# Performance work log

Hardware: AMD Instinct MI355X
Metric: run time of the kernel (lower is better)

The kernel has to match this reference:

```python
import jax, jax.numpy as jnp
import numpy as np

N = 50000      # nodes
E = 800000     # edges
NF = 128       # node_features
BF = 16        # bond_features
H = 4          # heads
C = 32         # hidden_size (per-head out channels)
HC = H * C     # 128 == NF, so all GAT layers share weight shape
DEPTH = 5
NEG_SLOPE = 0.2


def _sanitize(t):
    return jnp.nan_to_num(t, nan=0.0, posinf=1000.0, neginf=-1000.0)


def setup_inputs() -> dict:
    key = jax.random.key(0)
    ks = jax.random.split(key, 12)
    s = 0.1
    x = jax.random.normal(ks[0], (N, NF), jnp.float32)
    edge_index = jax.random.randint(ks[1], (2, E), 0, N, dtype=jnp.int32)
    edge_attr = jax.random.uniform(ks[2], (E, BF), jnp.float32)
    W = jax.random.normal(ks[3], (DEPTH, NF, HC), jnp.float32) * s
    att_src = jax.random.normal(ks[4], (DEPTH, H, C), jnp.float32) * s
    att_dst = jax.random.normal(ks[5], (DEPTH, H, C), jnp.float32) * s
    We = jax.random.normal(ks[6], (DEPTH, BF, HC), jnp.float32) * s
    att_edge = jax.random.normal(ks[7], (DEPTH, H, C), jnp.float32) * s
    b = jnp.zeros((DEPTH, HC), jnp.float32)
    Wout = jax.random.normal(ks[8], (NF + HC, C), jnp.float32) * s
    bout = jnp.zeros((C,), jnp.float32)
    return {"x": x, "edge_index": edge_index, "edge_attr": edge_attr,
            "W": W, "att_src": att_src, "att_dst": att_dst,
            "We": We, "att_edge": att_edge, "b": b,
            "Wout": Wout, "bout": bout}


def _gat_layer(h, s2, d2, ea, W_l, as_l, ad_l, We_l, ae_l, b_l):
    # h: [N, in_dim]; s2/d2: [E+N] edges incl. self loops; ea: [E+N, BF]
    xp = (h @ W_l).reshape(N, H, C)                     # lin(x), view per-head
    a_s = jnp.sum(xp * as_l, axis=-1)                   # [N, H]
    a_d = jnp.sum(xp * ad_l, axis=-1)                   # [N, H]
    ee = (ea @ We_l).reshape(-1, H, C)                  # lin_edge(edge_attr)
    a_e = jnp.sum(ee * ae_l, axis=-1)                   # [E+N, H]
    alpha = jax.nn.leaky_relu(a_s[s2] + a_d[d2] + a_e, NEG_SLOPE)
    # segment softmax over edges grouped by destination node
    m = jax.ops.segment_max(alpha, d2, num_segments=N)  # every node has a self loop -> finite
    ex = jnp.exp(alpha - m[d2])
    den = jax.ops.segment_sum(ex, d2, num_segments=N)
    coef = ex / (den[d2] + 1e-16)                       # [E+N, H]
    out = jax.ops.segment_sum(coef[:, :, None] * xp[s2], d2, num_segments=N)
    return out.reshape(N, HC) + b_l


def reference(x, edge_index, edge_attr, W, att_src, att_dst, We, att_edge, b, Wout, bout):
    src, dst = edge_index[0], edge_index[1]
    # add self loops with fill_value='mean': self-loop attr = mean of incoming edge_attr
    deg = jax.ops.segment_sum(jnp.ones((E,), edge_attr.dtype), dst, num_segments=N)
    sl_attr = jax.ops.segment_sum(edge_attr, dst, num_segments=N) / jnp.maximum(deg, 1.0)[:, None]
    ea = jnp.concatenate([edge_attr, sl_attr], axis=0)          # [E+N, BF]
    loop = jnp.arange(N, dtype=src.dtype)
    s2 = jnp.concatenate([src, loop])
    d2 = jnp.concatenate([dst, loop])

    h = _sanitize(x)
    for l in range(DEPTH):
        h = _gat_layer(h, s2, d2, ea, W[l], att_src[l], att_dst[l], We[l], att_edge[l], b[l])
        h = jax.nn.relu(h)            # dropout is a no-op in eval mode
        h = _sanitize(h)
    h_cat = jnp.concatenate([x, h], axis=1)             # [N, NF+HC]
    out = jax.nn.relu(h_cat @ Wout + bout)
    return _sanitize(out)
```

## Files before the change

### kernel.cpp

```cpp
#include <hip/hip_runtime.h>

#define NN 50000
#define NE 800000
#define NF 128
#define BF 16
#define NH 4
#define HC 128
#define CC 32
#define DEPTH 5
#define NEG 0.2f
#define NPART 256
#define PTILE 4096

typedef __attribute__((ext_vector_type(8))) short bf16x8;
typedef __attribute__((ext_vector_type(4))) float f32x4;

__device__ inline unsigned short f2bf(float f) {
  union { float f; unsigned u; } v; v.f = f;
  unsigned r = v.u + 0x7fff + ((v.u >> 16) & 1);
  return (unsigned short)(r >> 16);
}
__device__ inline float bf2f(unsigned short u) {
  union { unsigned u; float f; } v; v.u = (unsigned)u << 16; return v.f;
}

__global__ void k_count(const int* __restrict__ dst, int* __restrict__ deg) {
  int e = blockIdx.x * 256 + threadIdx.x;
  if (e < NE) atomicAdd(&deg[dst[e]], 1);
}

__global__ void k_partial(const int* __restrict__ deg, int* __restrict__ bsum) {
  __shared__ int s[256];
  int t = threadIdx.x;
  int i = blockIdx.x * 256 + t;
  s[t] = (i < NN) ? deg[i] : 0;
  __syncthreads();
  for (int d = 128; d > 0; d >>= 1) {
    if (t < d) s[t] += s[t + d];
    __syncthreads();
  }
  if (t == 0) bsum[blockIdx.x] = s[0];
}

__global__ void k_scan_top(int* __restrict__ bsum, int nb) {
  if (threadIdx.x == 0 && blockIdx.x == 0) {
    int run = 0;
    for (int i = 0; i < nb; ++i) { int v = bsum[i]; bsum[i] = run; run += v; }
  }
}

__global__ void k_scan_write(const int* __restrict__ deg, const int* __restrict__ bsum,
                             int* __restrict__ offs) {
  __shared__ int s[256];
  int t = threadIdx.x;
  int i = blockIdx.x * 256 + t;
  int v = (i < NN) ? deg[i] : 0;
  s[t] = v;
  __syncthreads();
  for (int d = 1; d < 256; d <<= 1) {
    int x = (t >= d) ? s[t - d] : 0;
    __syncthreads();
    s[t] += x;
    __syncthreads();
  }
  if (i < NN) offs[i] = bsum[blockIdx.x] + s[t] - v;
  if (i == 0) offs[NN] = NE;
}

__global__ void k_initcur(const int* __restrict__ offs, int* __restrict__ cur) {
  int i = blockIdx.x * 256 + threadIdx.x;
  if (i < NN) cur[i] = offs[i];
}

__global__ __launch_bounds__(256) void k_p0(const int* __restrict__ edst, int* __restrict__ pcnt) {
  __shared__ int lc[NPART];
  int t = threadIdx.x;
  lc[t] = 0;
  __syncthreads();
  int base = blockIdx.x * PTILE;
#pragma unroll
  for (int j = 0; j < PTILE / 256; ++j) {
    int e = base + t + j * 256;
    if (e < NE) atomicAdd(&lc[edst[e] >> 8], 1);
  }
  __syncthreads();
  if (lc[t]) atomicAdd(&pcnt[t], lc[t]);
}

__global__ void k_pscan(const int* __restrict__ pcnt, int* __restrict__ pbase,
                        int* __restrict__ pcur) {
  __shared__ int s[NPART];
  int t = threadIdx.x;
  int v = pcnt[t];
  s[t] = v;
  __syncthreads();
  for (int d = 1; d < NPART; d <<= 1) {
    int x = (t >= d) ? s[t - d] : 0;
    __syncthreads();
    s[t] += x;
    __syncthreads();
  }
  int ex = s[t] - v;
  pbase[t] = ex;
  pcur[t] = ex;
  if (t == NPART - 1) pbase[NPART] = s[NPART - 1];
}

__global__ __launch_bounds__(256) void k_p1(const int* __restrict__ edst,
                                            int* __restrict__ pcur,
                                            int2* __restrict__ staging) {
  __shared__ int lc[NPART];
  __shared__ int lbase[NPART];
  __shared__ int lrank[NPART];
  int t = threadIdx.x;
  lc[t] = 0;
  __syncthreads();
  int base = blockIdx.x * PTILE;
  int myd[PTILE / 256];
#pragma unroll
  for (int j = 0; j < PTILE / 256; ++j) {
    int e = base + t + j * 256;
    int d = (e < NE) ? edst[e] : -1;
    myd[j] = d;
    if (d >= 0) atomicAdd(&lc[d >> 8], 1);
  }
  __syncthreads();
  if (lc[t]) lbase[t] = atomicAdd(&pcur[t], lc[t]);
  lrank[t] = 0;
  __syncthreads();
#pragma unroll
  for (int j = 0; j < PTILE / 256; ++j) {
    int d = myd[j];
    if (d >= 0) {
      int p = d >> 8;
      int r = atomicAdd(&lrank[p], 1);
      staging[lbase[p] + r] = make_int2(base + t + j * 256, d);
    }
  }
}

__global__ __launch_bounds__(256) void k_p2(const int2* __restrict__ staging,
                                            const int* __restrict__ pbase,
                                            int* __restrict__ cur,
                                            int* __restrict__ csr_eid) {
  int p = blockIdx.x;
  int s = pbase[p], e = pbase[p + 1];
  for (int i = s + threadIdx.x; i < e; i += 256) {
    int2 st = staging[i];
    int slot = atomicAdd(&cur[st.y], 1);
    csr_eid[slot] = st.x;
  }
}

__global__ void k_weff(const float* __restrict__ We, const float* __restrict__ ae,
                       float* __restrict__ weff) {
  int idx = threadIdx.x;
  if (idx >= DEPTH * BF * NH) return;
  int l = idx / (BF * NH);
  int r = idx - l * (BF * NH);
  int f = r >> 2, h = r & 3;
  const float* We_l = We + (size_t)l * BF * HC;
  const float* ae_l = ae + (size_t)l * NH * CC;
  float acc = 0.f;
  for (int c = 0; c < CC; ++c) acc += We_l[f * HC + h * CC + c] * ae_l[h * CC + c];
  weff[idx] = acc;
}

__global__ __launch_bounds__(256) void k_aeprep(const int* __restrict__ csr_eid,
                                                const int* __restrict__ esrc,
                                                const float* __restrict__ eattr,
                                                const float* __restrict__ weff,
                                                unsigned short* __restrict__ ae_csr,
                                                int* __restrict__ csr_src) {
  __shared__ float sw[DEPTH * BF * NH];
  int t = threadIdx.x;
  if (t < DEPTH * BF * NH) sw[t] = weff[t];
  __syncthreads();
  int i = blockIdx.x * 256 + t;
  if (i >= NE) return;
  int eid = csr_eid[i];
  csr_src[i] = esrc[eid];
  float at[16];
  const float4* ar = (const float4*)(eattr + (size_t)eid * BF);
#pragma unroll
  for (int q = 0; q < 4; ++q) {
    float4 v = ar[q];
    at[q * 4] = v.x; at[q * 4 + 1] = v.y; at[q * 4 + 2] = v.z; at[q * 4 + 3] = v.w;
  }
#pragma unroll
  for (int l = 0; l < DEPTH; ++l) {
    float a0 = 0.f, a1 = 0.f, a2 = 0.f, a3 = 0.f;
#pragma unroll
    for (int f = 0; f < BF; ++f) {
      float av = at[f];
      const float* wf = &sw[(l * BF + f) * NH];
      a0 += av * wf[0]; a1 += av * wf[1]; a2 += av * wf[2]; a3 += av * wf[3];
    }
    ushort4 u;
    u.x = f2bf(a0); u.y = f2bf(a1); u.z = f2bf(a2); u.w = f2bf(a3);
    ((ushort4*)ae_csr)[(size_t)l * NE + i] = u;
  }
}

__global__ void k_aeself(const unsigned short* __restrict__ ae_csr,
                         const int* __restrict__ offs,
                         unsigned short* __restrict__ ae_self) {
  int idx = blockIdx.x * 256 + threadIdx.x;
  if (idx >= NN * DEPTH) return;
  int l = idx / NN, n = idx - l * NN;
  int s = offs[n], e = offs[n + 1];
  const ushort4* base = (const ushort4*)ae_csr + (size_t)l * NE;
  float a0 = 0.f, a1 = 0.f, a2 = 0.f, a3 = 0.f;
  for (int i = s; i < e; ++i) {
    ushort4 u = base[i];
    a0 += bf2f(u.x); a1 += bf2f(u.y); a2 += bf2f(u.z); a3 += bf2f(u.w);
  }
  float inv = 1.0f / fmaxf((float)(e - s), 1.0f);
  ushort4 o;
  o.x = f2bf(a0 * inv); o.y = f2bf(a1 * inv); o.z = f2bf(a2 * inv); o.w = f2bf(a3 * inv);
  ((ushort4*)ae_self)[(size_t)l * NN + n] = o;
}

__global__ void k_x2bf(const float* __restrict__ x, unsigned short* __restrict__ xb) {
  int i = blockIdx.x * 256 + threadIdx.x;
  if (i >= NN * 32) return;
  float4 v = ((const float4*)x)[i];
  ushort4 u;
  u.x = f2bf(v.x); u.y = f2bf(v.y); u.z = f2bf(v.z); u.w = f2bf(v.w);
  ((ushort4*)xb)[i] = u;
}

__global__ void k_wprep(const float* __restrict__ W, unsigned short* __restrict__ Wt) {
  int idx = blockIdx.x * 256 + threadIdx.x;
  if (idx >= DEPTH * NF * HC) return;
  int l = idx >> 14;
  int rem = idx & 16383;
  int n = rem >> 7, k = rem & 127;
  Wt[(size_t)l * 16384 + (size_t)n * 128 + k] = f2bf(W[(size_t)l * 16384 + (size_t)k * 128 + n]);
}

__global__ __launch_bounds__(256) void k_gemm_mfma(const unsigned short* __restrict__ Ab,
                                                   const unsigned short* __restrict__ Wt,
                                                   const float* __restrict__ as_w,
                                                   const float* __restrict__ ad_w,
                                                   unsigned short* __restrict__ xpb,
                                                   float* __restrict__ a_s,
                                                   float* __restrict__ a_d) {
  __shared__ unsigned short cl[64][144];
  __shared__ float swS[128], dwS[128];
  int t = threadIdx.x;
  if (t < 128) { swS[t] = as_w[t]; dwS[t] = ad_w[t]; }
  int wv = t >> 6;
  int l = t & 63;
  int r0 = blockIdx.x * 64;
  int lk = (l >> 4) * 8;
  int c0 = wv * 32;
  f32x4 acc[4][2] = {};
#pragma unroll
  for (int ks = 0; ks < 4; ++ks) {
    int kb = ks * 32 + lk;
    bf16x8 bfr0 = *(const bf16x8*)&Wt[(size_t)(c0 + (l & 15)) * 128 + kb];
    bf16x8 bfr1 = *(const bf16x8*)&Wt[(size_t)(c0 + 16 + (l & 15)) * 128 + kb];
#pragma unroll
    for (int rt = 0; rt < 4; ++rt) {
      int row = r0 + rt * 16 + (l & 15);
      row = row < NN ? row : NN - 1;
      bf16x8 afr = *(const bf16x8*)&Ab[(size_t)row * 128 + kb];
      acc[rt][0] = __builtin_amdgcn_mfma_f32_16x16x32_bf16(afr, bfr0, acc[rt][0], 0, 0, 0);
      acc[rt][1] = __builtin_amdgcn_mfma_f32_16x16x32_bf16(afr, bfr1, acc[rt][1], 0, 0, 0);
    }
  }
#pragma unroll
  for (int rt = 0; rt < 4; ++rt) {
#pragma unroll
    for (int j = 0; j < 4; ++j) {
      int lr = rt * 16 + (l >> 4) * 4 + j;
      cl[lr][c0 + (l & 15)] = f2bf(acc[rt][0][j]);
      cl[lr][c0 + 16 + (l & 15)] = f2bf(acc[rt][1][j]);
    }
  }
  __syncthreads();
  int row = t >> 2;
  int grow = r0 + row;
  int p = t & 3;
  if (grow < NN) {
    uint4* dst = (uint4*)&xpb[(size_t)grow * 128];
#pragma unroll
    for (int q = 0; q < 4; ++q)
      dst[q * 4 + p] = *(uint4*)&cl[row][(q * 4 + p) * 8];
  }
  int hh = t & 3;
  int hc = hh * 32;
  float ps = 0.f, pd = 0.f;
#pragma unroll
  for (int q = 0; q < 4; ++q) {
    uint4 u = *(uint4*)&cl[row][hc + q * 8];
    const unsigned short* us = (const unsigned short*)&u;
#pragma unroll
    for (int k = 0; k < 8; ++k) {
      float xv = bf2f(us[k]);
      ps += xv * swS[hc + q * 8 + k];
      pd += xv * dwS[hc + q * 8 + k];
    }
  }
  if (grow < NN) {
    a_s[(size_t)grow * 4 + hh] = ps;
    a_d[(size_t)grow * 4 + hh] = pd;
  }
}

__global__ __launch_bounds__(256) void k_aggr(const unsigned short* __restrict__ xpb,
                                              const unsigned short* __restrict__ ae_l,
                                              const unsigned short* __restrict__ aeself_l,
                                              const float* __restrict__ a_s,
                                              const float* __restrict__ a_d,
                                              const int* __restrict__ csr_src,
                                              const int* __restrict__ offs,
                                              const float* __restrict__ b_l,
                                              unsigned short* __restrict__ hout) {
  int node = blockIdx.x * 4 + (threadIdx.x >> 6);
  if (node >= NN) return;
  int lane = threadIdx.x & 63;
  int q = lane & 15;
  int h = lane >> 4;
  int base = lane & 48;
  const ushort2* xp2 = (const ushort2*)xpb;
  int s = offs[node], e = offs[node + 1];
  float ad = a_d[(size_t)node * 4 + h];
  float vs = a_s[(size_t)node * 4 + h] + ad + bf2f(aeself_l[(size_t)node * 4 + h]);
  vs = vs > 0.f ? vs : NEG * vs;
  float es = __expf(fminf(vs, 60.f));
  ushort2 xs = xp2[(size_t)node * 64 + lane];
  float acc0 = es * bf2f(xs.x), acc1 = es * bf2f(xs.y);
  float den = es;
  for (int i = s; i < e; i += 16) {
    int cnt = e - i;
    int srcv = 0;
    float w = 0.f;
    if (q < cnt) {
      srcv = csr_src[i + q];
      float a = a_s[(size_t)srcv * 4 + h] + ad + bf2f(ae_l[(size_t)(i + q) * 4 + h]);
      a = a > 0.f ? a : NEG * a;
      w = __expf(fminf(a, 60.f));
    }
#pragma unroll 8
    for (int qq = 0; qq < 16; ++qq) {
      int sq = __shfl(srcv, base | qq);
      float wq = __shfl(w, base | qq);
      ushort2 xq = xp2[(size_t)sq * 64 + lane];
      den += wq;
      acc0 += wq * bf2f(xq.x);
      acc1 += wq * bf2f(xq.y);
    }
  }
  float2 b2 = ((const float2*)b_l)[lane];
  float inv = 1.0f / (den + 1e-16f);
  float o0 = fmaxf(acc0 * inv + b2.x, 0.f);
  float o1 = fmaxf(acc1 * inv + b2.y, 0.f);
  ushort2 ho;
  ho.x = f2bf(o0); ho.y = f2bf(o1);
  ((ushort2*)hout)[(size_t)node * 64 + lane] = ho;
}

__global__ __launch_bounds__(256) void k_final(const float* __restrict__ x,
                                               const unsigned short* __restrict__ h,
                                               const float* __restrict__ Wout, const float* __restrict__ bout,
                                               float* __restrict__ out) {
  __shared__ float4 wlds[2048];
  int t = threadIdx.x;
#pragma unroll
  for (int i = 0; i < 8; ++i) wlds[t + i * 256] = ((const float4*)Wout)[t + i * 256];
  __syncthreads();
  int tx = t & 7;
  int ty = t >> 3;
  int row0 = blockIdx.x * 64 + ty;
  int row1 = row0 + 32;
  bool v0 = row0 < NN, v1 = row1 < NN;
  const float4* x4 = (const float4*)x;
  const ushort4* h4 = (const ushort4*)h;
  float acc[2][4] = {};
  const float4 z = make_float4(0.f, 0.f, 0.f, 0.f);
#pragma unroll 4
  for (int k4 = 0; k4 < 32; ++k4) {
    float4 a0 = v0 ? x4[(size_t)row0 * 32 + k4] : z;
    float4 a1 = v1 ? x4[(size_t)row1 * 32 + k4] : z;
    float av0[4] = {a0.x, a0.y, a0.z, a0.w};
    float av1[4] = {a1.x, a1.y, a1.z, a1.w};
#pragma unroll
    for (int kk = 0; kk < 4; ++kk) {
      float4 w = wlds[(k4 * 4 + kk) * 8 + tx];
      acc[0][0] += av0[kk] * w.x; acc[0][1] += av0[kk] * w.y;
      acc[0][2] += av0[kk] * w.z; acc[0][3] += av0[kk] * w.w;
      acc[1][0] += av1[kk] * w.x; acc[1][1] += av1[kk] * w.y;
      acc[1][2] += av1[kk] * w.z; acc[1][3] += av1[kk] * w.w;
    }
  }
#pragma unroll 4
  for (int k4 = 0; k4 < 32; ++k4) {
    ushort4 u0 = v0 ? h4[(size_t)row0 * 32 + k4] : make_ushort4(0, 0, 0, 0);
    ushort4 u1 = v1 ? h4[(size_t)row1 * 32 + k4] : make_ushort4(0, 0, 0, 0);
    float av0[4] = {bf2f(u0.x), bf2f(u0.y), bf2f(u0.z), bf2f(u0.w)};
    float av1[4] = {bf2f(u1.x), bf2f(u1.y), bf2f(u1.z), bf2f(u1.w)};
#pragma unroll
    for (int kk = 0; kk < 4; ++kk) {
      float4 w = wlds[(128 + k4 * 4 + kk) * 8 + tx];
      acc[0][0] += av0[kk] * w.x; acc[0][1] += av0[kk] * w.y;
      acc[0][2] += av0[kk] * w.z; acc[0][3] += av0[kk] * w.w;
      acc[1][0] += av1[kk] * w.x; acc[1][1] += av1[kk] * w.y;
      acc[1][2] += av1[kk] * w.z; acc[1][3] += av1[kk] * w.w;
    }
  }
  float4 b4 = ((const float4*)bout)[tx];
  if (v0) {
    float4 o = make_float4(fmaxf(acc[0][0] + b4.x, 0.f), fmaxf(acc[0][1] + b4.y, 0.f),
                           fmaxf(acc[0][2] + b4.z, 0.f), fmaxf(acc[0][3] + b4.w, 0.f));
    ((float4*)out)[(size_t)row0 * 8 + tx] = o;
  }
  if (v1) {
    float4 o = make_float4(fmaxf(acc[1][0] + b4.x, 0.f), fmaxf(acc[1][1] + b4.y, 0.f),
                           fmaxf(acc[1][2] + b4.z, 0.f), fmaxf(acc[1][3] + b4.w, 0.f));
    ((float4*)out)[(size_t)row1 * 8 + tx] = o;
  }
}

extern "C" void kernel_launch(void* const* d_in, const int* in_sizes, int n_in,
                              void* d_out, int out_size, void* d_ws, size_t ws_size,
                              hipStream_t stream) {
  const float* x        = (const float*)d_in[0];
  const int*   eidx     = (const int*)d_in[1];
  const float* eattr    = (const float*)d_in[2];
  const float* W        = (const float*)d_in[3];
  const float* att_src  = (const float*)d_in[4];
  const float* att_dst  = (const float*)d_in[5];
  const float* We       = (const float*)d_in[6];
  const float* att_edge = (const float*)d_in[7];
  const float* b        = (const float*)d_in[8];
  const float* Wout     = (const float*)d_in[9];
  const float* bout     = (const float*)d_in[10];
  float* out = (float*)d_out;

  const int* esrc = eidx;
  const int* edst = eidx + NE;

  size_t off = 0;
  auto carve = [&](size_t bytes) {
    void* p = (char*)d_ws + off;
    off += (bytes + 255) & ~(size_t)255;
    return p;
  };
  unsigned short* h_buf   = (unsigned short*)carve((size_t)NN * HC * 2);
  unsigned short* xpb     = (unsigned short*)carve((size_t)NN * HC * 2);
  unsigned short* Wt      = (unsigned short*)carve((size_t)DEPTH * NF * HC * 2);
  unsigned short* ae_csr  = (unsigned short*)carve((size_t)DEPTH * NE * NH * 2);
  unsigned short* ae_self = (unsigned short*)carve((size_t)DEPTH * NN * NH * 2);
  float* a_s   = (float*)carve((size_t)NN * NH * 4);
  float* a_d   = (float*)carve((size_t)NN * NH * 4);
  float* weff  = (float*)carve((size_t)DEPTH * BF * NH * 4);
  int* deg  = (int*)carve((size_t)NN * 4);
  int* offs = (int*)carve((size_t)(NN + 1) * 4);
  int* cur  = (int*)carve((size_t)NN * 4);
  int2* staging = (int2*)carve((size_t)NE * 8);
  int* csr_eid = (int*)carve((size_t)NE * 4);
  int* csr_src = (int*)carve((size_t)NE * 4);
  int* pcnt  = (int*)carve((size_t)NPART * 4);
  int* pbase = (int*)carve((size_t)(NPART + 1) * 4);
  int* pcur  = (int*)carve((size_t)NPART * 4);
  int* bsum = (int*)carve(1024);

  const int nbN = (NN + 255) / 256;
  const int nbE = (NE + 255) / 256;
  const int nbP = (NE + PTILE - 1) / PTILE;

  hipMemsetAsync(deg, 0, (size_t)NN * 4, stream);
  hipMemsetAsync(pcnt, 0, (size_t)NPART * 4, stream);
  k_count<<<nbE, 256, 0, stream>>>(edst, deg);
  k_partial<<<nbN, 256, 0, stream>>>(deg, bsum);
  k_scan_top<<<1, 64, 0, stream>>>(bsum, nbN);
  k_scan_write<<<nbN, 256, 0, stream>>>(deg, bsum, offs);
  k_initcur<<<nbN, 256, 0, stream>>>(offs, cur);
  k_p0<<<nbP, 256, 0, stream>>>(edst, pcnt);
  k_pscan<<<1, NPART, 0, stream>>>(pcnt, pbase, pcur);
  k_p1<<<nbP, 256, 0, stream>>>(edst, pcur, staging);
  k_p2<<<NPART, 256, 0, stream>>>(staging, pbase, cur, csr_eid);
  k_weff<<<1, 320, 0, stream>>>(We, att_edge, weff);
  k_aeprep<<<nbE, 256, 0, stream>>>(csr_eid, esrc, eattr, weff, ae_csr, csr_src);
  k_aeself<<<(NN * DEPTH + 255) / 256, 256, 0, stream>>>(ae_csr, offs, ae_self);
  k_x2bf<<<(NN * 32 + 255) / 256, 256, 0, stream>>>(x, h_buf);
  k_wprep<<<(DEPTH * NF * HC + 255) / 256, 256, 0, stream>>>(W, Wt);

  for (int l = 0; l < DEPTH; ++l) {
    k_gemm_mfma<<<(NN + 63) / 64, 256, 0, stream>>>(h_buf, Wt + (size_t)l * NF * HC,
                                                    att_src + (size_t)l * NH * CC,
                                                    att_dst + (size_t)l * NH * CC,
                                                    xpb, a_s, a_d);
    k_aggr<<<(NN + 3) / 4, 256, 0, stream>>>(xpb,
                                             ae_csr + (size_t)l * NE * NH,
                                             ae_self + (size_t)l * NN * NH,
                                             a_s, a_d, csr_src, offs,
                                             b + (size_t)l * HC, h_buf);
  }
  k_final<<<(NN + 63) / 64, 256, 0, stream>>>(x, h_buf, Wout, bout, out);
}
```

Measured before the change: 484.0 us.

## Fuse CSR setup kernels, enlarge GEMM row tile, add nontemporal loads/stores in aggregation

Merges the degree count and partition histogram into one pass over destinations, and folds the cur initialisation into the scan-write kernel, which removes two launches and one read of the edge array. The MFMA GEMM now handles 128 rows per block instead of 64, reusing the weight fragments across more rows at the cost of more accumulator registers and LDS. The aggregation kernel uses nontemporal loads for the streamed CSR source and edge-attention arrays and a nontemporal packed store for the output, so that streaming data pollutes the cache less.

```diff
diff --git a/kernel.cpp b/kernel.cpp
--- a/kernel.cpp
+++ b/kernel.cpp
@@ -24,9 +24,25 @@
   union { unsigned u; float f; } v; v.u = (unsigned)u << 16; return v.f;
 }
 
-__global__ void k_count(const int* __restrict__ dst, int* __restrict__ deg) {
-  int e = blockIdx.x * 256 + threadIdx.x;
-  if (e < NE) atomicAdd(&deg[dst[e]], 1);
+__global__ __launch_bounds__(256) void k_cnt0(const int* __restrict__ edst,
+                                              int* __restrict__ deg,
+                                              int* __restrict__ pcnt) {
+  __shared__ int lc[NPART];
+  int t = threadIdx.x;
+  lc[t] = 0;
+  __syncthreads();
+  int base = blockIdx.x * PTILE;
+#pragma unroll
+  for (int j = 0; j < PTILE / 256; ++j) {
+    int e = base + t + j * 256;
+    if (e < NE) {
+      int d = edst[e];
+      atomicAdd(&deg[d], 1);
+      atomicAdd(&lc[d >> 8], 1);
+    }
+  }
+  __syncthreads();
+  if (lc[t]) atomicAdd(&pcnt[t], lc[t]);
 }
 
 __global__ void k_partial(const int* __restrict__ deg, int* __restrict__ bsum) {
@@ -50,7 +66,7 @@
 }
 
 __global__ void k_scan_write(const int* __restrict__ deg, const int* __restrict__ bsum,
-                             int* __restrict__ offs) {
+                             int* __restrict__ offs, int* __restrict__ cur) {
   __shared__ int s[256];
   int t = threadIdx.x;
   int i = blockIdx.x * 256 + t;
@@ -63,28 +79,12 @@
     s[t] += x;
     __syncthreads();
   }
-  if (i < NN) offs[i] = bsum[blockIdx.x] + s[t] - v;
+  if (i < NN) {
+    int o = bsum[blockIdx.x] + s[t] - v;
+    offs[i] = o;
+    cur[i] = o;
+  }
   if (i == 0) offs[NN] = NE;
-}
-
-__global__ void k_initcur(const int* __restrict__ offs, int* __restrict__ cur) {
-  int i = blockIdx.x * 256 + threadIdx.x;
-  if (i < NN) cur[i] = offs[i];
-}
-
-__global__ __launch_bounds__(256) void k_p0(const int* __restrict__ edst, int* __restrict__ pcnt) {
-  __shared__ int lc[NPART];
-  int t = threadIdx.x;
-  lc[t] = 0;
-  __syncthreads();
-  int base = blockIdx.x * PTILE;
-#pragma unroll
-  for (int j = 0; j < PTILE / 256; ++j) {
-    int e = base + t + j * 256;
-    if (e < NE) atomicAdd(&lc[edst[e] >> 8], 1);
-  }
-  __syncthreads();
-  if (lc[t]) atomicAdd(&pcnt[t], lc[t]);
 }
 
 __global__ void k_pscan(const int* __restrict__ pcnt, int* __restrict__ pbase,
@@ -246,23 +246,23 @@
                                                    unsigned short* __restrict__ xpb,
                                                    float* __restrict__ a_s,
                                                    float* __restrict__ a_d) {
-  __shared__ unsigned short cl[64][144];
+  __shared__ unsigned short cl[128][144];
   __shared__ float swS[128], dwS[128];
   int t = threadIdx.x;
   if (t < 128) { swS[t] = as_w[t]; dwS[t] = ad_w[t]; }
   int wv = t >> 6;
   int l = t & 63;
-  int r0 = blockIdx.x * 64;
+  int r0 = blockIdx.x * 128;
   int lk = (l >> 4) * 8;
   int c0 = wv * 32;
-  f32x4 acc[4][2] = {};
+  f32x4 acc[8][2] = {};
 #pragma unroll
   for (int ks = 0; ks < 4; ++ks) {
     int kb = ks * 32 + lk;
     bf16x8 bfr0 = *(const bf16x8*)&Wt[(size_t)(c0 + (l & 15)) * 128 + kb];
     bf16x8 bfr1 = *(const bf16x8*)&Wt[(size_t)(c0 + 16 + (l & 15)) * 128 + kb];
 #pragma unroll
-    for (int rt = 0; rt < 4; ++rt) {
+    for (int rt = 0; rt < 8; ++rt) {
       int row = r0 + rt * 16 + (l & 15);
       row = row < NN ? row : NN - 1;
       bf16x8 afr = *(const bf16x8*)&Ab[(size_t)row * 128 + kb];
@@ -271,7 +271,7 @@
     }
   }
 #pragma unroll
-  for (int rt = 0; rt < 4; ++rt) {
+  for (int rt = 0; rt < 8; ++rt) {
 #pragma unroll
     for (int j = 0; j < 4; ++j) {
       int lr = rt * 16 + (l >> 4) * 4 + j;
@@ -280,32 +280,38 @@
     }
   }
   __syncthreads();
-  int row = t >> 2;
+  int row = t >> 1;
   int grow = r0 + row;
-  int p = t & 3;
+  int p = t & 1;
   if (grow < NN) {
     uint4* dst = (uint4*)&xpb[(size_t)grow * 128];
 #pragma unroll
-    for (int q = 0; q < 4; ++q)
-      dst[q * 4 + p] = *(uint4*)&cl[row][(q * 4 + p) * 8];
-  }
+    for (int q = 0; q < 8; ++q)
+      dst[q * 2 + p] = *(uint4*)&cl[row][(q * 2 + p) * 8];
+  }
+  int row2 = t >> 2;
   int hh = t & 3;
   int hc = hh * 32;
-  float ps = 0.f, pd = 0.f;
-#pragma unroll
-  for (int q = 0; q < 4; ++q) {
-    uint4 u = *(uint4*)&cl[row][hc + q * 8];
-    const unsigned short* us = (const unsigned short*)&u;
-#pragma unroll
-    for (int k = 0; k < 8; ++k) {
-      float xv = bf2f(us[k]);
-      ps += xv * swS[hc + q * 8 + k];
-      pd += xv * dwS[hc + q * 8 + k];
-    }
-  }
-  if (grow < NN) {
-    a_s[(size_t)grow * 4 + hh] = ps;
-    a_d[(size_t)grow * 4 + hh] = pd;
+#pragma unroll
+  for (int half = 0; half < 2; ++half) {
+    int rr = row2 + half * 64;
+    int gr = r0 + rr;
+    float ps = 0.f, pd = 0.f;
+#pragma unroll
+    for (int q = 0; q < 4; ++q) {
+      uint4 u = *(uint4*)&cl[rr][hc + q * 8];
+      const unsigned short* us = (const unsigned short*)&u;
+#pragma unroll
+      for (int k = 0; k < 8; ++k) {
+        float xv = bf2f(us[k]);
+        ps += xv * swS[hc + q * 8 + k];
+        pd += xv * dwS[hc + q * 8 + k];
+      }
+    }
+    if (gr < NN) {
+      a_s[(size_t)gr * 4 + hh] = ps;
+      a_d[(size_t)gr * 4 + hh] = pd;
+    }
   }
 }
 
@@ -338,8 +344,9 @@
     int srcv = 0;
     float w = 0.f;
     if (q < cnt) {
-      srcv = csr_src[i + q];
-      float a = a_s[(size_t)srcv * 4 + h] + ad + bf2f(ae_l[(size_t)(i + q) * 4 + h]);
+      srcv = __builtin_nontemporal_load(&csr_src[i + q]);
+      unsigned short aeu = __builtin_nontemporal_load(&ae_l[(size_t)(i + q) * 4 + h]);
+      float a = a_s[(size_t)srcv * 4 + h] + ad + bf2f(aeu);
       a = a > 0.f ? a : NEG * a;
       w = __expf(fminf(a, 60.f));
     }
@@ -357,9 +364,8 @@
   float inv = 1.0f / (den + 1e-16f);
   float o0 = fmaxf(acc0 * inv + b2.x, 0.f);
   float o1 = fmaxf(acc1 * inv + b2.y, 0.f);
-  ushort2 ho;
-  ho.x = f2bf(o0); ho.y = f2bf(o1);
-  ((ushort2*)hout)[(size_t)node * 64 + lane] = ho;
+  unsigned int packed = (unsigned int)f2bf(o0) | ((unsigned int)f2bf(o1) << 16);
+  __builtin_nontemporal_store(packed, &((unsigned int*)hout)[(size_t)node * 64 + lane]);
 }
 
 __global__ __launch_bounds__(256) void k_final(const float* __restrict__ x,
@@ -473,12 +479,10 @@
 
   hipMemsetAsync(deg, 0, (size_t)NN * 4, stream);
   hipMemsetAsync(pcnt, 0, (size_t)NPART * 4, stream);
-  k_count<<<nbE, 256, 0, stream>>>(edst, deg);
+  k_cnt0<<<nbP, 256, 0, stream>>>(edst, deg, pcnt);
   k_partial<<<nbN, 256, 0, stream>>>(deg, bsum);
   k_scan_top<<<1, 64, 0, stream>>>(bsum, nbN);
-  k_scan_write<<<nbN, 256, 0, stream>>>(deg, bsum, offs);
-  k_initcur<<<nbN, 256, 0, stream>>>(offs, cur);
-  k_p0<<<nbP, 256, 0, stream>>>(edst, pcnt);
+  k_scan_write<<<nbN, 256, 0, stream>>>(deg, bsum, offs, cur);
   k_pscan<<<1, NPART, 0, stream>>>(pcnt, pbase, pcur);
   k_p1<<<nbP, 256, 0, stream>>>(edst, pcur, staging);
   k_p2<<<NPART, 256, 0, stream>>>(staging, pbase, cur, csr_eid);
@@ -489,10 +493,10 @@
   k_wprep<<<(DEPTH * NF * HC + 255) / 256, 256, 0, stream>>>(W, Wt);
 
   for (int l = 0; l < DEPTH; ++l) {
-    k_gemm_mfma<<<(NN + 63) / 64, 256, 0, stream>>>(h_buf, Wt + (size_t)l * NF * HC,
-                                                    att_src + (size_t)l * NH * CC,
-                                                    att_dst + (size_t)l * NH * CC,
-                                                    xpb, a_s, a_d);
+    k_gemm_mfma<<<(NN + 127) / 128, 256, 0, stream>>>(h_buf, Wt + (size_t)l * NF * HC,
+                                                      att_src + (size_t)l * NH * CC,
+                                                      att_dst + (size_t)l * NH * CC,
+                                                      xpb, a_s, a_d);
     k_aggr<<<(NN + 3) / 4, 256, 0, stream>>>(xpb,
                                              ae_csr + (size_t)l * NE * NH,
                                              ae_self + (size_t)l * NN * NH,
```

Measured after the change: 503.5 us. +4.0%, slower.
